# Optimization experiments

Measured on AMD Instinct MI355X. Metric: run time of the kernel, lower is better.

The kernel has to match this reference:

```python
import jax, jax.numpy as jnp
import numpy as np

D_MODEL = 1024  # scale uses sqrt(d_model), matching the source's sqrt(C)

def setup_inputs() -> dict:
    key = jax.random.key(0)
    kx, kq, kk, kv = jax.random.split(key, 4)
    B, T, C, H = 8, 2048, D_MODEL, 64
    s = 1.0 / np.sqrt(C)
    return {
        "x": jax.random.normal(kx, (B, T, C), dtype=jnp.float32),
        "Wq": jax.random.normal(kq, (C, H), dtype=jnp.float32) * s,
        "Wk": jax.random.normal(kk, (C, H), dtype=jnp.float32) * s,
        "Wv": jax.random.normal(kv, (C, H), dtype=jnp.float32) * s,
    }

def reference(x, Wq, Wk, Wv):
    B, T, C = x.shape
    q = jnp.einsum("btc,ch->bth", x, Wq)
    k = jnp.einsum("btc,ch->bth", x, Wk)
    v = jnp.einsum("btc,ch->bth", x, Wv)
    # scores scaled by 1/sqrt(C) (C = d_model), faithful to source
    wei = jnp.einsum("bth,bsh->bts", q, k) / jnp.sqrt(jnp.float32(C))
    causal = jnp.tril(jnp.ones((T, T), dtype=bool))  # [T, T]
    wei = jnp.where(causal, wei, -jnp.inf)
    wei = jax.nn.softmax(wei, axis=-1)
    out = jnp.einsum("bts,bsh->bth", wei, v)
    return out
```

## Files before the change

kernel.cpp:

```cpp
#include <hip/hip_runtime.h>

typedef unsigned short u16;
typedef __attribute__((ext_vector_type(4))) float f32x4;
typedef __attribute__((ext_vector_type(8))) short bf16x8;
typedef __attribute__((ext_vector_type(4))) u16 u16x4;
typedef __attribute__((ext_vector_type(8))) u16 u16x8;

#define MFMA(a, b, c) __builtin_amdgcn_mfma_f32_16x16x32_bf16(a, b, c, 0, 0, 0)

__device__ __forceinline__ u16 f2bf(float f) {
    unsigned u = __float_as_uint(f);
    u += 0x7fffu + ((u >> 16) & 1u);
    return (u16)(u >> 16);
}
__device__ __forceinline__ float bf2f(u16 h) {
    unsigned u = ((unsigned)h) << 16;
    return __uint_as_float(u);
}

__device__ __forceinline__ void load_lds16(const void* g, void* l) {
    __builtin_amdgcn_global_load_lds((const __attribute__((address_space(1))) void*)g,
                                     (__attribute__((address_space(3))) void*)l,
                                     16, 0, 0);
}

__global__ void wt_pack(const float* __restrict__ Wq, const float* __restrict__ Wk,
                        const float* __restrict__ Wv, u16* __restrict__ Wtt) {
    const int k = blockIdx.x;
    const int n = threadIdx.x;
    const float* W = (n < 64) ? Wq : (n < 128 ? Wk : Wv);
    const float v = W[(size_t)k * 64 + (n & 63)];
    const int mat = n >> 6, nl = n & 63;
    const int kt = k >> 6, ks = k & 63, c = ks >> 3, ci = ks & 7;
    Wtt[(size_t)((mat * 16 + kt) * 64 + nl) * 64 + (((c ^ (nl & 7)) << 3) + ci)] = f2bf(v);
}

__global__ __launch_bounds__(256, 3) void qkv_gemm(const float* __restrict__ x,
                                                   const u16* __restrict__ Wtt,
                                                   u16* __restrict__ qo,
                                                   u16* __restrict__ ko,
                                                   u16* __restrict__ vT) {
    const int tid = threadIdx.x;
    const int lane = tid & 63, wave = tid >> 6;
    const int lr = lane & 15, lg = lane >> 4;
    const int mat = blockIdx.x >> 8;
    const int m0 = (blockIdx.x & 255) * 64;

    __shared__ __align__(16) float xs[2][64 * 64];
    __shared__ __align__(16) u16 ws[2][64 * 64];

    f32x4 acc[4];
#pragma unroll
    for (int m = 0; m < 4; ++m) acc[m] = (f32x4){0.f, 0.f, 0.f, 0.f};

#define QSTAGE(bufi, kt_)                                                               \
    {                                                                                   \
        _Pragma("unroll") for (int j = 0; j < 4; ++j) {                                 \
            const int cid = j * 256 + tid;                                              \
            const int row = cid >> 4, cc = cid & 15;                                    \
            load_lds16(x + (size_t)(m0 + row) * 1024 + (kt_)*64 +                       \
                           ((cc ^ (row & 7)) << 2),                                     \
                       &xs[bufi][(j * 256 + wave * 64) * 4]);                           \
        }                                                                               \
        _Pragma("unroll") for (int j = 0; j < 2; ++j) {                                 \
            const int cid = j * 256 + tid;                                              \
            load_lds16(Wtt + (size_t)(mat * 16 + (kt_)) * 4096 + cid * 8,               \
                       &ws[bufi][(j * 256 + wave * 64) * 8]);                           \
        }                                                                               \
    }

    QSTAGE(0, 0);
    __syncthreads();

    for (int kt = 0; kt < 16; ++kt) {
        const int cur = kt & 1;
        if (kt < 15) QSTAGE(cur ^ 1, kt + 1);

#pragma unroll
        for (int h = 0; h < 2; ++h) {
            const int wrow = wave * 16 + lr;
            const int cb = h * 4 + lg;
            const bf16x8 b = *(const bf16x8*)&ws[cur][wrow * 64 + ((cb ^ (wrow & 7)) << 3)];
#pragma unroll
            for (int mm = 0; mm < 4; ++mm) {
                const int rr = mm * 16 + lr;
                const int c0 = h * 8 + lg * 2;
                f32x4 f0 = *(const f32x4*)&xs[cur][rr * 64 + ((c0 ^ (rr & 7)) << 2)];
                f32x4 f1 = *(const f32x4*)&xs[cur][rr * 64 + (((c0 + 1) ^ (rr & 7)) << 2)];
                bf16x8 a;
#pragma unroll
                for (int i = 0; i < 4; ++i) {
                    a[i] = (short)f2bf(f0[i]);
                    a[i + 4] = (short)f2bf(f1[i]);
                }
                acc[mm] = MFMA(a, b, acc[mm]);
            }
        }
        __syncthreads();
    }

    const float SCQ = 0.0450842200277801f;
    const int col = wave * 16 + lr;
    if (mat == 0) {
#pragma unroll
        for (int mm = 0; mm < 4; ++mm) {
            const int rl = m0 + mm * 16 + lg * 4;
#pragma unroll
            for (int r = 0; r < 4; ++r)
                qo[(size_t)(rl + r) * 64 + col] = f2bf(acc[mm][r] * SCQ);
        }
    } else if (mat == 1) {
#pragma unroll
        for (int mm = 0; mm < 4; ++mm) {
            const int rl = m0 + mm * 16 + lg * 4;
#pragma unroll
            for (int r = 0; r < 4; ++r)
                ko[(size_t)(rl + r) * 64 + col] = f2bf(acc[mm][r]);
        }
    } else {
        const int bb = m0 >> 11;
        const int tb = m0 & 2047;
#pragma unroll
        for (int mm = 0; mm < 4; ++mm) {
            u16x4 pk;
#pragma unroll
            for (int r = 0; r < 4; ++r) pk[r] = f2bf(acc[mm][r]);
            *(u16x4*)&vT[(size_t)(bb * 64 + col) * 2048 + tb + mm * 16 + lg * 4] = pk;
        }
    }
}

#define PPITCH 72
__global__ __launch_bounds__(256, 3) void attn_part(const u16* __restrict__ q,
                                                    const u16* __restrict__ k,
                                                    const u16* __restrict__ vT,
                                                    u16* __restrict__ Opb,
                                                    float* __restrict__ Lp) {
    const int b = blockIdx.x & 7;
    int g = blockIdx.x >> 3;
    int qt = 31, rem = g;
    while (rem >= (qt >> 3) + 1) { rem -= (qt >> 3) + 1; --qt; }
    const int c0 = rem;
    const int q0 = qt * 64;
    const int kv_lo = c0 * 512;
    const int kv_hi = min(kv_lo + 512, q0 + 64);
    const int ntiles = (kv_hi - kv_lo) >> 6;
    const int slot = (b * 32 + qt) * 4 + c0;

    __shared__ __align__(16) u16 lK[2][64 * 64];
    __shared__ __align__(16) u16 lV[2][64 * 64];
    __shared__ __align__(16) u16 lP[4][16 * PPITCH];

    const int tid = threadIdx.x;
    const int wave = tid >> 6, lane = tid & 63;
    const int lr = lane & 15, lg = lane >> 4;

    const u16* qb = q + (size_t)b * 2048 * 64;
    const u16* kb = k + (size_t)b * 2048 * 64;
    const u16* vb = vT + (size_t)b * 64 * 2048;

    const int myrow = q0 + wave * 16 + lr;
    const bf16x8 qf0 = *(const bf16x8*)(qb + (size_t)myrow * 64 + lg * 8);
    const bf16x8 qf1 = *(const bf16x8*)(qb + (size_t)myrow * 64 + 32 + lg * 8);

    f32x4 oacc[4];
#pragma unroll
    for (int n = 0; n < 4; ++n) oacc[n] = (f32x4){0.f, 0.f, 0.f, 0.f};
    float rs = 0.f;

#define ASTAGE(bufi, kv0_)                                                             \
    {                                                                                  \
        _Pragma("unroll") for (int j = 0; j < 2; ++j) {                                \
            const int cid = j * 256 + wave * 64 + lane;                                \
            const int row = cid >> 3, cc = cid & 7;                                    \
            load_lds16(kb + (size_t)((kv0_) + row) * 64 + ((cc ^ (row & 7)) << 3),     \
                       &lK[bufi][(j * 256 + wave * 64) * 8]);                          \
            load_lds16(vb + (size_t)row * 2048 + (kv0_) + ((cc ^ (row & 7)) << 3),     \
                       &lV[bufi][(j * 256 + wave * 64) * 8]);                          \
        }                                                                              \
    }

    ASTAGE(0, kv_lo);
    __syncthreads();

    for (int it = 0; it < ntiles; ++it) {
        const int cur = it & 1;
        if (it + 1 < ntiles) ASTAGE(cur ^ 1, kv_lo + (it + 1) * 64);

        const int kv0 = kv_lo + it * 64;
        if (kv0 <= q0 + wave * 16 + 15) {
            f32x4 s[4];
            __builtin_amdgcn_s_setprio(1);
#pragma unroll
            for (int n = 0; n < 4; ++n) {
                const int row = n * 16 + lr;
                const bf16x8 kf0 = *(const bf16x8*)&lK[cur][row * 64 + ((lg ^ (row & 7)) << 3)];
                const bf16x8 kf1 =
                    *(const bf16x8*)&lK[cur][row * 64 + (((4 + lg) ^ (row & 7)) << 3)];
                f32x4 a = (f32x4){0.f, 0.f, 0.f, 0.f};
                a = MFMA(kf0, qf0, a);
                a = MFMA(kf1, qf1, a);
                s[n] = a;
            }
            __builtin_amdgcn_s_setprio(0);

            const bool msk = (kv0 + 63 > q0 + wave * 16);
#pragma unroll
            for (int n = 0; n < 4; ++n) {
                u16x4 pk;
#pragma unroll
                for (int r = 0; r < 4; ++r) {
                    const int kvi = kv0 + n * 16 + lg * 4 + r;
                    const float p = (!msk || kvi <= myrow) ? exp2f(s[n][r]) : 0.f;
                    rs += p;
                    pk[r] = f2bf(p);
                }
                *(u16x4*)&lP[wave][lr * PPITCH + n * 16 + lg * 4] = pk;
            }

            __builtin_amdgcn_s_setprio(1);
#pragma unroll
            for (int kc = 0; kc < 2; ++kc) {
                const bf16x8 pf = *(const bf16x8*)&lP[wave][lr * PPITCH + kc * 32 + lg * 8];
#pragma unroll
                for (int n = 0; n < 4; ++n) {
                    const int row = n * 16 + lr;
                    const bf16x8 vf =
                        *(const bf16x8*)&lV[cur][row * 64 + (((kc * 4 + lg) ^ (row & 7)) << 3)];
                    oacc[n] = MFMA(pf, vf, oacc[n]);
                }
            }
            __builtin_amdgcn_s_setprio(0);
        }
        __syncthreads();
    }

    rs += __shfl_xor(rs, 16);
    rs += __shfl_xor(rs, 32);
    if (lane < 16) Lp[slot * 64 + wave * 16 + lr] = rs;

    u16* op = Opb + (size_t)slot * 4096 + wave * 1024;
#pragma unroll
    for (int n = 0; n < 4; ++n)
#pragma unroll
        for (int r = 0; r < 4; ++r)
            op[n * 256 + (lg * 4 + r) * 16 + lr] = f2bf(oacc[n][r]);
}

__global__ __launch_bounds__(256) void attn_combine(const u16* __restrict__ Opb,
                                                    const float* __restrict__ Lp,
                                                    float* __restrict__ out) {
    const int gid = blockIdx.x * 256 + threadIdx.x;
    const int colg = gid & 7;
    const int row = gid >> 3;
    const int b = row >> 11, tt = row & 2047;
    const int qt = tt >> 6, i = tt & 63;
    const int nc = (qt >> 3) + 1;
    const size_t sbase = (size_t)(b * 32 + qt) * 4;
    const int sub0 = (i >> 4) * 1024 + (colg >> 1) * 256 + (i & 15) * 16 + (colg & 1) * 8;

    float O[8] = {0.f, 0.f, 0.f, 0.f, 0.f, 0.f, 0.f, 0.f};
    float L = 0.f;
    for (int c = 0; c < nc; ++c) {
        const u16x8 v = *(const u16x8*)&Opb[(sbase + c) * 4096 + sub0];
#pragma unroll
        for (int j = 0; j < 8; ++j) O[j] += bf2f(v[j]);
        L += Lp[(sbase + c) * 64 + i];
    }
    const float rinv = 1.0f / L;
    f32x4 o0, o1;
#pragma unroll
    for (int j = 0; j < 4; ++j) {
        o0[j] = O[j] * rinv;
        o1[j] = O[4 + j] * rinv;
    }
    float* ob = out + (size_t)row * 64 + colg * 8;
    *(f32x4*)(ob) = o0;
    *(f32x4*)(ob + 4) = o1;
}

extern "C" void kernel_launch(void* const* d_in, const int* in_sizes, int n_in,
                              void* d_out, int out_size, void* d_ws, size_t ws_size,
                              hipStream_t stream) {
    const float* x = (const float*)d_in[0];
    const float* Wq = (const float*)d_in[1];
    const float* Wk = (const float*)d_in[2];
    const float* Wv = (const float*)d_in[3];
    float* out = (float*)d_out;

    char* ws = (char*)d_ws;
    u16* Wtt = (u16*)ws;
    u16* qb = (u16*)(ws + (512 << 10));
    u16* kb = (u16*)(ws + (512 << 10) + (2 << 20));
    u16* vT = (u16*)(ws + (512 << 10) + (4 << 20));
    u16* Opb = (u16*)(ws + (8 << 20));
    float* Lp = (float*)(ws + (20 << 20));

    wt_pack<<<1024, 192, 0, stream>>>(Wq, Wk, Wv, Wtt);
    qkv_gemm<<<768, 256, 0, stream>>>(x, Wtt, qb, kb, vT);
    attn_part<<<640, 256, 0, stream>>>(qb, kb, vT, Opb, Lp);
    attn_combine<<<512, 256, 0, stream>>>(Opb, Lp, out);
}
```

Before: 60.42 us.

## Fuse Q/K/V projections into one block reading x once, weights held in registers

The QKV GEMM now uses 768-thread blocks over 32-row tiles, and each block computes all three projections (192 output columns). Before, three separate 64x64 blocks each reloaded the same x tile, so x was read from global memory three times; now it is read once. Weights are repacked column-major and loaded straight from global into registers in two halves instead of being staged through LDS. This cuts x traffic and LDS weight traffic, at the cost of more registers per thread and fewer MFMAs per x-tile load.

```diff
diff --git a/kernel.cpp b/kernel.cpp
--- a/kernel.cpp
+++ b/kernel.cpp
@@ -24,108 +24,109 @@
                                      16, 0, 0);
 }
 
-__global__ void wt_pack(const float* __restrict__ Wq, const float* __restrict__ Wk,
-                        const float* __restrict__ Wv, u16* __restrict__ Wtt) {
-    const int k = blockIdx.x;
-    const int n = threadIdx.x;
+__global__ __launch_bounds__(256) void wt_pack(const float* __restrict__ Wq,
+                                               const float* __restrict__ Wk,
+                                               const float* __restrict__ Wv,
+                                               u16* __restrict__ Wt2) {
+    const int n = blockIdx.x;
+    const int t = threadIdx.x;
     const float* W = (n < 64) ? Wq : (n < 128 ? Wk : Wv);
-    const float v = W[(size_t)k * 64 + (n & 63)];
-    const int mat = n >> 6, nl = n & 63;
-    const int kt = k >> 6, ks = k & 63, c = ks >> 3, ci = ks & 7;
-    Wtt[(size_t)((mat * 16 + kt) * 64 + nl) * 64 + (((c ^ (nl & 7)) << 3) + ci)] = f2bf(v);
-}
-
-__global__ __launch_bounds__(256, 3) void qkv_gemm(const float* __restrict__ x,
-                                                   const u16* __restrict__ Wtt,
+    const int c = n & 63;
+    u16x4 pk;
+#pragma unroll
+    for (int i = 0; i < 4; ++i) pk[i] = f2bf(W[(size_t)(t * 4 + i) * 64 + c]);
+    *(u16x4*)&Wt2[(size_t)n * 1024 + t * 4] = pk;
+}
+
+__global__ __launch_bounds__(768, 3) void qkv_gemm(const float* __restrict__ x,
+                                                   const u16* __restrict__ Wt2,
                                                    u16* __restrict__ qo,
                                                    u16* __restrict__ ko,
                                                    u16* __restrict__ vT) {
     const int tid = threadIdx.x;
     const int lane = tid & 63, wave = tid >> 6;
     const int lr = lane & 15, lg = lane >> 4;
-    const int mat = blockIdx.x >> 8;
-    const int m0 = (blockIdx.x & 255) * 64;
-
-    __shared__ __align__(16) float xs[2][64 * 64];
-    __shared__ __align__(16) u16 ws[2][64 * 64];
-
-    f32x4 acc[4];
-#pragma unroll
-    for (int m = 0; m < 4; ++m) acc[m] = (f32x4){0.f, 0.f, 0.f, 0.f};
-
-#define QSTAGE(bufi, kt_)                                                               \
-    {                                                                                   \
-        _Pragma("unroll") for (int j = 0; j < 4; ++j) {                                 \
-            const int cid = j * 256 + tid;                                              \
-            const int row = cid >> 4, cc = cid & 15;                                    \
-            load_lds16(x + (size_t)(m0 + row) * 1024 + (kt_)*64 +                       \
-                           ((cc ^ (row & 7)) << 2),                                     \
-                       &xs[bufi][(j * 256 + wave * 64) * 4]);                           \
-        }                                                                               \
-        _Pragma("unroll") for (int j = 0; j < 2; ++j) {                                 \
-            const int cid = j * 256 + tid;                                              \
-            load_lds16(Wtt + (size_t)(mat * 16 + (kt_)) * 4096 + cid * 8,               \
-                       &ws[bufi][(j * 256 + wave * 64) * 8]);                           \
-        }                                                                               \
+    const int m0 = blockIdx.x * 32;
+    const int colg = wave * 16 + lr;
+
+    __shared__ __align__(16) float xs[2][32 * 64];
+
+    f32x4 acc[2];
+    acc[0] = (f32x4){0.f, 0.f, 0.f, 0.f};
+    acc[1] = (f32x4){0.f, 0.f, 0.f, 0.f};
+
+#define QSTAGE(bufi, kg_)                                                              \
+    if (tid < 512) {                                                                   \
+        const int row = tid >> 4, cc = tid & 15;                                       \
+        load_lds16(x + (size_t)(m0 + row) * 1024 + (kg_)*64 + ((cc ^ (row & 7)) << 2), \
+                   &xs[bufi][wave * 256]);                                             \
     }
 
     QSTAGE(0, 0);
     __syncthreads();
 
-    for (int kt = 0; kt < 16; ++kt) {
-        const int cur = kt & 1;
-        if (kt < 15) QSTAGE(cur ^ 1, kt + 1);
-
-#pragma unroll
-        for (int h = 0; h < 2; ++h) {
-            const int wrow = wave * 16 + lr;
-            const int cb = h * 4 + lg;
-            const bf16x8 b = *(const bf16x8*)&ws[cur][wrow * 64 + ((cb ^ (wrow & 7)) << 3)];
-#pragma unroll
-            for (int mm = 0; mm < 4; ++mm) {
-                const int rr = mm * 16 + lr;
-                const int c0 = h * 8 + lg * 2;
-                f32x4 f0 = *(const f32x4*)&xs[cur][rr * 64 + ((c0 ^ (rr & 7)) << 2)];
-                f32x4 f1 = *(const f32x4*)&xs[cur][rr * 64 + (((c0 + 1) ^ (rr & 7)) << 2)];
-                bf16x8 a;
-#pragma unroll
-                for (int i = 0; i < 4; ++i) {
-                    a[i] = (short)f2bf(f0[i]);
-                    a[i + 4] = (short)f2bf(f1[i]);
+    const u16* wcol = Wt2 + (size_t)colg * 1024 + lg * 8;
+
+#pragma unroll
+    for (int p = 0; p < 2; ++p) {
+        bf16x8 bfr[8][2];
+#pragma unroll
+        for (int kt = 0; kt < 8; ++kt)
+#pragma unroll
+            for (int h = 0; h < 2; ++h)
+                bfr[kt][h] = *(const bf16x8*)(wcol + p * 512 + kt * 64 + h * 32);
+
+#pragma unroll
+        for (int kt = 0; kt < 8; ++kt) {
+            const int kg = p * 8 + kt;
+            const int cur = kg & 1;
+            if (kg < 15) QSTAGE(cur ^ 1, kg + 1);
+
+#pragma unroll
+            for (int h = 0; h < 2; ++h) {
+#pragma unroll
+                for (int mm = 0; mm < 2; ++mm) {
+                    const int rr = mm * 16 + lr;
+                    const int c0 = h * 8 + lg * 2;
+                    f32x4 f0 = *(const f32x4*)&xs[cur][rr * 64 + ((c0 ^ (rr & 7)) << 2)];
+                    f32x4 f1 = *(const f32x4*)&xs[cur][rr * 64 + (((c0 + 1) ^ (rr & 7)) << 2)];
+                    bf16x8 a;
+#pragma unroll
+                    for (int i = 0; i < 4; ++i) {
+                        a[i] = (short)f2bf(f0[i]);
+                        a[i + 4] = (short)f2bf(f1[i]);
+                    }
+                    acc[mm] = MFMA(a, bfr[kt][h], acc[mm]);
                 }
-                acc[mm] = MFMA(a, b, acc[mm]);
             }
+            __syncthreads();
         }
-        __syncthreads();
     }
 
     const float SCQ = 0.0450842200277801f;
-    const int col = wave * 16 + lr;
-    if (mat == 0) {
-#pragma unroll
-        for (int mm = 0; mm < 4; ++mm) {
-            const int rl = m0 + mm * 16 + lg * 4;
+    const int bb = m0 >> 11;
+    const int tb = m0 & 2047;
+    if (colg < 64) {
+#pragma unroll
+        for (int mm = 0; mm < 2; ++mm)
 #pragma unroll
             for (int r = 0; r < 4; ++r)
-                qo[(size_t)(rl + r) * 64 + col] = f2bf(acc[mm][r] * SCQ);
-        }
-    } else if (mat == 1) {
-#pragma unroll
-        for (int mm = 0; mm < 4; ++mm) {
-            const int rl = m0 + mm * 16 + lg * 4;
+                qo[(size_t)(m0 + mm * 16 + lg * 4 + r) * 64 + colg] =
+                    f2bf(acc[mm][r] * SCQ);
+    } else if (colg < 128) {
+#pragma unroll
+        for (int mm = 0; mm < 2; ++mm)
 #pragma unroll
             for (int r = 0; r < 4; ++r)
-                ko[(size_t)(rl + r) * 64 + col] = f2bf(acc[mm][r]);
-        }
+                ko[(size_t)(m0 + mm * 16 + lg * 4 + r) * 64 + (colg - 64)] =
+                    f2bf(acc[mm][r]);
     } else {
-        const int bb = m0 >> 11;
-        const int tb = m0 & 2047;
-#pragma unroll
-        for (int mm = 0; mm < 4; ++mm) {
+#pragma unroll
+        for (int mm = 0; mm < 2; ++mm) {
             u16x4 pk;
 #pragma unroll
             for (int r = 0; r < 4; ++r) pk[r] = f2bf(acc[mm][r]);
-            *(u16x4*)&vT[(size_t)(bb * 64 + col) * 2048 + tb + mm * 16 + lg * 4] = pk;
+            *(u16x4*)&vT[(size_t)(bb * 64 + (colg - 128)) * 2048 + tb + mm * 16 + lg * 4] = pk;
         }
     }
 }
@@ -289,15 +290,15 @@
     float* out = (float*)d_out;
 
     char* ws = (char*)d_ws;
-    u16* Wtt = (u16*)ws;
+    u16* Wt2 = (u16*)ws;
     u16* qb = (u16*)(ws + (512 << 10));
     u16* kb = (u16*)(ws + (512 << 10) + (2 << 20));
     u16* vT = (u16*)(ws + (512 << 10) + (4 << 20));
     u16* Opb = (u16*)(ws + (8 << 20));
     float* Lp = (float*)(ws + (20 << 20));
 
-    wt_pack<<<1024, 192, 0, stream>>>(Wq, Wk, Wv, Wtt);
-    qkv_gemm<<<768, 256, 0, stream>>>(x, Wtt, qb, kb, vT);
+    wt_pack<<<192, 256, 0, stream>>>(Wq, Wk, Wv, Wt2);
+    qkv_gemm<<<512, 768, 0, stream>>>(x, Wt2, qb, kb, vT);
     attn_part<<<640, 256, 0, stream>>>(qb, kb, vT, Opb, Lp);
     attn_combine<<<512, 256, 0, stream>>>(Opb, Lp, out);
 }
```

Result: slower. 75.89 us (+25.6%).
